# Kernel tuning notes

Hardware: AMD Instinct MI355X
Metric: run time of the kernel (lower is better)

The kernel has to match this reference:

```python
import jax, jax.numpy as jnp
import numpy as np

EPS = 1e-12

def _safe_norm(x, axis):
    return jnp.sqrt(jnp.sum(x * x, axis=axis) + EPS)

def _forward(z, pos, edge_index, batch, batch_size, emb, centers, gamma,
             fw1, fb1, fw2, fb2, uw1, ub1, uw2, ub2,
             ew1, eb1, ew2, eb2, dipole_w, nac_w,
             aw1, ab1, aw2, ab2, yw1, yb1, yw2, yb2):
    row, col = edge_index[0], edge_index[1]
    N = pos.shape[0]
    diff = pos[col] - pos[row]                    # (E,3)
    dist = _safe_norm(diff, axis=1)               # (E,)
    dirs = diff / (dist[:, None] + 1e-8)          # (E,3)
    rbf = jnp.exp(-gamma * (dist[:, None] - centers) ** 2)   # (E,R)
    s = emb[z]                                    # (N,F)
    v = jnp.zeros((N, s.shape[1], 3), s.dtype)    # (N,F,3)
    n_layers = fw1.shape[0]
    for l in range(n_layers):
        # filter MLP on RBF features -> 3 gates per edge
        phi = jax.nn.silu(rbf @ fw1[l] + fb1[l]) @ fw2[l] + fb2[l]   # (E,3F)
        phi_ss, phi_vv, phi_sv = jnp.split(phi, 3, axis=-1)
        sc = s[col]                                                    # gather (E,F)
        m_s = jax.ops.segment_sum(phi_ss * sc, row, num_segments=N)    # (N,F)
        m_v_e = (phi_vv[..., None] * v[col]
                 + phi_sv[..., None] * dirs[:, None, :] * sc[..., None])  # (E,F,3)
        m_v = jax.ops.segment_sum(m_v_e, row, num_segments=N)          # (N,F,3)
        v_norm = _safe_norm(m_v, axis=-1)                              # (N,F)
        upd = (jax.nn.silu(jnp.concatenate([s, m_s, v_norm], axis=-1) @ uw1[l] + ub1[l])
               @ uw2[l] + ub2[l])                                       # (N,3F)
        delta_s, alpha, beta = jnp.split(upd, 3, axis=-1)
        s = s + delta_s
        v = alpha[..., None] * v + beta[..., None] * m_v
    # energy heads (stacked over states S)
    h = jax.nn.silu(jnp.einsum('nf,sfg->nsg', s, ew1) + eb1)           # (N,S,F)
    e_atom = (jnp.einsum('nsg,sgo->nso', h, ew2) + eb2)[..., 0]        # (N,S)
    energies = jax.ops.segment_sum(e_atom, batch, num_segments=batch_size)  # (M,S)
    dipoles = jax.ops.segment_sum(jnp.einsum('nfk,f->nk', v, dipole_w), batch,
                                  num_segments=batch_size)             # (M,3)
    nac = jax.ops.segment_sum(jnp.einsum('nfk,pf->npk', v, nac_w), batch,
                              num_segments=batch_size)                 # (M,P,3)
    gaps = energies[:, 1:] - energies[:, :1]                           # (M,S-1)
    lam = jax.nn.silu(gaps @ aw1 + ab1) @ aw2 + ab2                    # (M,1)
    nac_mag = _safe_norm(nac, axis=-1)                                 # (M,P)
    phi_y = jax.nn.sigmoid(
        jax.nn.silu(jnp.concatenate([gaps, nac_mag], axis=1) @ yw1 + yb1) @ yw2 + yb2)  # (M,1)
    return energies, dipoles, nac, lam, phi_y

N, E, F, R, L, S, M, A = 20000, 320000, 128, 20, 3, 4, 1000, 100
P = S - 1

def setup_inputs() -> dict:
    key = jax.random.key(0)
    ks = jax.random.split(key, 32)
    w = lambda i, shape, sc=0.05: jax.random.normal(ks[i], shape, jnp.float32) * sc
    return {
        'z': jax.random.randint(ks[0], (N,), 0, A),
        'pos': jax.random.normal(ks[1], (N, 3), jnp.float32),
        'edge_index': jax.random.randint(ks[2], (2, E), 0, N),
        'batch': jnp.sort(jax.random.randint(ks[3], (N,), 0, M)),
        'batch_size': M,
        'emb': jax.random.normal(ks[4], (A, F), jnp.float32),
        'centers': jnp.linspace(0.0, 5.0, R),
        'gamma': jnp.ones((R,), jnp.float32),
        'fw1': w(5, (L, R, F)), 'fb1': jnp.zeros((L, F)),
        'fw2': w(6, (L, F, 3 * F)), 'fb2': jnp.zeros((L, 3 * F)),
        'uw1': w(7, (L, 3 * F, F)), 'ub1': jnp.zeros((L, F)),
        'uw2': w(8, (L, F, 3 * F)), 'ub2': jnp.zeros((L, 3 * F)),
        'ew1': w(9, (S, F, F)), 'eb1': jnp.zeros((S, F)),
        'ew2': w(10, (S, F, 1)), 'eb2': jnp.zeros((S, 1)),
        'dipole_w': jax.random.normal(ks[11], (F,), jnp.float32),
        'nac_w': jax.random.normal(ks[12], (P, F), jnp.float32),
        'aw1': w(13, (S - 1, 64)), 'ab1': jnp.zeros((64,)),
        'aw2': w(14, (64, 1)), 'ab2': jnp.zeros((1,)),
        'yw1': w(15, (S - 1 + P, 128)), 'yb1': jnp.zeros((128,)),
        'yw2': w(16, (128, 1)), 'yb2': jnp.zeros((1,)),
    }

def reference(z, pos, edge_index, batch, batch_size, emb, centers, gamma,
              fw1, fb1, fw2, fb2, uw1, ub1, uw2, ub2,
              ew1, eb1, ew2, eb2, dipole_w, nac_w,
              aw1, ab1, aw2, ab2, yw1, yb1, yw2, yb2):
    return _forward(z, pos, edge_index, batch, batch_size, emb, centers, gamma,
                    fw1, fb1, fw2, fb2, uw1, ub1, uw2, ub2,
                    ew1, eb1, ew2, eb2, dipole_w, nac_w,
                    aw1, ab1, aw2, ab2, yw1, yb1, yw2, yb2)
```

## Files before the change

kernel.cpp:

```cpp
#include <hip/hip_runtime.h>
#include <hip/hip_fp16.h>

#define FDIM 128
#define RDIM 20

#define TAB_T 2048
#define TAB_RANGE 12.0f

constexpr int TH = 256;

__device__ __forceinline__ float siluf(float x) { return x / (1.f + __expf(-x)); }

__device__ __forceinline__ void store_h4(__half* p, float a, float b, float c, float d) {
    __half h[4] = {__float2half(a), __float2half(b), __float2half(c), __float2half(d)};
    *(uint2*)p = *(uint2*)h;
}

__global__ void k_init(const int* __restrict__ z, const float* __restrict__ emb,
                       float* __restrict__ s, __half* __restrict__ s_h, int N) {
    int i = blockIdx.x * blockDim.x + threadIdx.x;
    if (i >= N * FDIM) return;
    int n = i >> 7, f = i & 127;
    float val = emb[z[n] * FDIM + f];
    s[i] = val;
    s_h[i] = __float2half(val);
}

__global__ void k_hist(const int* __restrict__ erow, int* __restrict__ cursor, int E) {
    int e = blockIdx.x * blockDim.x + threadIdx.x;
    if (e < E) atomicAdd(&cursor[erow[e]], 1);
}

__global__ __launch_bounds__(256) void k_scan1(const int* __restrict__ cursor,
                                               int* __restrict__ rowstart,
                                               int* __restrict__ bsum, int N) {
    __shared__ int sh[256];
    int tid = threadIdx.x;
    int idx = blockIdx.x * 256 + tid;
    int x = (idx < N) ? cursor[idx] : 0;
    sh[tid] = x;
    __syncthreads();
    #pragma unroll
    for (int off = 1; off < 256; off <<= 1) {
        int t = (tid >= off) ? sh[tid - off] : 0;
        __syncthreads();
        sh[tid] += t;
        __syncthreads();
    }
    if (idx < N) rowstart[idx] = sh[tid] - x;
    if (tid == 255) bsum[blockIdx.x] = sh[255];
}

__global__ __launch_bounds__(256) void k_scan2(int* __restrict__ bsum,
                                               int* __restrict__ rowstart, int nb, int N) {
    __shared__ int sh[256];
    __shared__ int carry;
    int tid = threadIdx.x;
    if (tid == 0) carry = 0;
    __syncthreads();
    for (int base = 0; base < nb; base += 256) {
        int idx = base + tid;
        int x = (idx < nb) ? bsum[idx] : 0;
        sh[tid] = x;
        __syncthreads();
        #pragma unroll
        for (int off = 1; off < 256; off <<= 1) {
            int t = (tid >= off) ? sh[tid - off] : 0;
            __syncthreads();
            sh[tid] += t;
            __syncthreads();
        }
        if (idx < nb) bsum[idx] = carry + sh[tid] - x;
        __syncthreads();
        if (tid == 0) carry += sh[255];
        __syncthreads();
    }
    if (tid == 0) rowstart[N] = carry;
}

__global__ __launch_bounds__(256) void k_scan3(int* __restrict__ rowstart,
                                               int* __restrict__ cursor,
                                               const int* __restrict__ bsum, int N) {
    int idx = blockIdx.x * 256 + threadIdx.x;
    if (idx < N) {
        int val = rowstart[idx] + bsum[blockIdx.x];
        rowstart[idx] = val;
        cursor[idx] = val;
    }
}

__global__ void k_fill(const int* __restrict__ erow, int* __restrict__ cursor,
                       int* __restrict__ esort, int E) {
    int e = blockIdx.x * blockDim.x + threadIdx.x;
    if (e < E) {
        int p = atomicAdd(&cursor[erow[e]], 1);
        esort[p] = e;
    }
}

__global__ void k_geom(const float* __restrict__ pos, const int* __restrict__ erow,
                       const int* __restrict__ ecol, const int* __restrict__ esort,
                       int2* __restrict__ geo_ci, float4* __restrict__ geo_wd,
                       float inv_step, int E) {
    int i = blockIdx.x * blockDim.x + threadIdx.x;
    if (i >= E) return;
    int e  = esort[i];
    int rw = erow[e], cl = ecol[e];
    float dx = pos[cl*3+0] - pos[rw*3+0];
    float dy = pos[cl*3+1] - pos[rw*3+1];
    float dz = pos[cl*3+2] - pos[rw*3+2];
    float dist = sqrtf(dx*dx + dy*dy + dz*dz + 1e-12f);
    float inv = 1.f / (dist + 1e-8f);
    float u = fminf(dist * inv_step, (float)TAB_T);
    int t0 = min((int)u, TAB_T - 1);
    geo_ci[i] = make_int2(cl, t0);
    geo_wd[i] = make_float4(u - (float)t0, dx*inv, dy*inv, dz*inv);
}

__global__ __launch_bounds__(TH) void k_table(
    const float* __restrict__ centers, const float* __restrict__ gamma,
    const float* __restrict__ fw1b, const float* __restrict__ fb1b,
    const float* __restrict__ fw2b, const float* __restrict__ fb2b,
    __half* __restrict__ tabb, float step)
{
    __shared__ float sh_rbf[32][RDIM];
    __shared__ float sh_ht[FDIM][33];
    __shared__ float sh_w[32][3 * FDIM + 4];

    const int l   = blockIdx.y;
    const float* fw1 = fw1b + (size_t)l * RDIM * FDIM;
    const float* fb1 = fb1b + (size_t)l * FDIM;
    const float* fw2 = fw2b + (size_t)l * FDIM * 3 * FDIM;
    const float* fb2 = fb2b + (size_t)l * 3 * FDIM;
    __half* tab = tabb + (size_t)l * (TAB_T + 1) * 384;

    const int p0  = blockIdx.x * 32;
    const int tid = threadIdx.x;

    for (int i = tid; i < 32 * RDIM; i += TH) {
        int p = i / RDIM, r = i - p * RDIM;
        float d = (float)(p0 + p) * step - centers[r];
        sh_rbf[p][r] = __expf(-gamma[r] * d * d);
    }
    __syncthreads();
    for (int i = tid; i < 32 * FDIM; i += TH) {
        int p = i >> 7, f = i & 127;
        float acc = fb1[f];
        #pragma unroll
        for (int r = 0; r < RDIM; ++r) acc += sh_rbf[p][r] * fw1[r * FDIM + f];
        sh_ht[f][p] = siluf(acc);
    }

    const int eq = tid & 7;
    const int fq = tid >> 3;
    const int f0 = fq * 4;

    float pg[3][4][4];
    #pragma unroll
    for (int g3 = 0; g3 < 3; ++g3)
        #pragma unroll
        for (int ee = 0; ee < 4; ++ee)
            #pragma unroll
            for (int i = 0; i < 4; ++i) pg[g3][ee][i] = fb2[g3 * FDIM + f0 + i];

    const int kkr = tid >> 3;
    const int t8  = tid & 7;
    for (int kc = 0; kc < 4; ++kc) {
        __syncthreads();
        #pragma unroll
        for (int j = 0; j < 12; ++j) {
            int g = (t8 * 12 + j) * 4;
            float4 w4 = *(const float4*)&fw2[(size_t)(kc * 32 + kkr) * (3 * FDIM) + g];
            *(float4*)&sh_w[kkr][g] = w4;
        }
        __syncthreads();
        #pragma unroll 4
        for (int kk = 0; kk < 32; ++kk) {
            float hv[4];
            #pragma unroll
            for (int ee = 0; ee < 4; ++ee) hv[ee] = sh_ht[kc * 32 + kk][4 * eq + ee];
            #pragma unroll
            for (int g3 = 0; g3 < 3; ++g3) {
                float4 w4 = *(const float4*)&sh_w[kk][g3 * FDIM + f0];
                #pragma unroll
                for (int ee = 0; ee < 4; ++ee) {
                    pg[g3][ee][0] += hv[ee] * w4.x;
                    pg[g3][ee][1] += hv[ee] * w4.y;
                    pg[g3][ee][2] += hv[ee] * w4.z;
                    pg[g3][ee][3] += hv[ee] * w4.w;
                }
            }
        }
    }

    #pragma unroll
    for (int ee = 0; ee < 4; ++ee) {
        int pt = p0 + 4 * eq + ee;
        if (pt <= TAB_T) {
            #pragma unroll
            for (int g3 = 0; g3 < 3; ++g3)
                store_h4(&tab[(size_t)pt * 384 + g3 * FDIM + f0],
                         pg[g3][ee][0], pg[g3][ee][1], pg[g3][ee][2], pg[g3][ee][3]);
        }
    }
}

__global__ __launch_bounds__(256) void k_repack(const __half* __restrict__ tab,
                                                __half2* __restrict__ tab2) {
    int l = blockIdx.y;
    const __half* t  = tab  + (size_t)l * (TAB_T + 1) * 384;
    __half2*      t2 = tab2 + (size_t)l * TAB_T * 384;
    int i = blockIdx.x * 256 + threadIdx.x;
    t2[i] = __halves2half2(t[i], t[i + 384]);
}

__global__ __launch_bounds__(128) void k_gather(
    const int* __restrict__ rowstart,
    const int2* __restrict__ geo_ci, const float4* __restrict__ geo_wd,
    const __half2* __restrict__ tab2, const __half* __restrict__ s_h,
    const __half* __restrict__ v_h,
    __half* __restrict__ m_s_h, __half* __restrict__ vnorm_h, __half* __restrict__ m_v_h,
    int withv, int N)
{
    __shared__ int   sh_col[32];
    __shared__ int   sh_t0[32];
    __shared__ float sh_w[32];
    __shared__ float sh_d0[32], sh_d1[32], sh_d2[32];

    const int n   = blockIdx.x;
    const int tid = threadIdx.x;
    const int lo  = rowstart[n], hi = rowstart[n + 1];

    float acc_s = 0.f, av0 = 0.f, av1 = 0.f, av2 = 0.f;

    for (int base = lo; base < hi; base += 32) {
        const int ne = min(32, hi - base);
        __syncthreads();
        if (tid < 32) {
            int idx = base + tid;
            if (tid < ne) {
                int2   ci = geo_ci[idx];
                float4 wd = geo_wd[idx];
                sh_col[tid] = ci.x; sh_t0[tid] = ci.y;
                sh_w[tid] = wd.x;
                sh_d0[tid] = wd.y; sh_d1[tid] = wd.z; sh_d2[tid] = wd.w;
            } else {
                sh_col[tid] = 0; sh_t0[tid] = 0; sh_w[tid] = 0.f;
                sh_d0[tid] = sh_d1[tid] = sh_d2[tid] = 0.f;
            }
        }
        __syncthreads();
        if (withv) {
            #pragma unroll 2
            for (int el = 0; el < ne; ++el) {
                int   cl = sh_col[el];
                int   t0 = sh_t0[el];
                float w  = sh_w[el];
                const __half2* t2 = tab2 + (size_t)t0 * 384 + tid;
                float2 pss2 = __half22float2(t2[0]);
                float2 pvv2 = __half22float2(t2[128]);
                float2 psv2 = __half22float2(t2[256]);
                float pss = pss2.x + w * (pss2.y - pss2.x);
                float pvv = pvv2.x + w * (pvv2.y - pvv2.x);
                float psv = psv2.x + w * (psv2.y - psv2.x);
                float sc = __half2float(s_h[(size_t)cl * FDIM + tid]);
                const __half* vp = v_h + (size_t)cl * 3 * FDIM + tid;
                float svs = psv * sc;
                acc_s += pss * sc;
                av0 += pvv * __half2float(vp[0])        + svs * sh_d0[el];
                av1 += pvv * __half2float(vp[FDIM])     + svs * sh_d1[el];
                av2 += pvv * __half2float(vp[2*FDIM])   + svs * sh_d2[el];
            }
        } else {
            #pragma unroll 2
            for (int el = 0; el < ne; ++el) {
                int   cl = sh_col[el];
                int   t0 = sh_t0[el];
                float w  = sh_w[el];
                const __half2* t2 = tab2 + (size_t)t0 * 384 + tid;
                float2 pss2 = __half22float2(t2[0]);
                float2 psv2 = __half22float2(t2[256]);
                float pss = pss2.x + w * (pss2.y - pss2.x);
                float psv = psv2.x + w * (psv2.y - psv2.x);
                float sc = __half2float(s_h[(size_t)cl * FDIM + tid]);
                float svs = psv * sc;
                acc_s += pss * sc;
                av0 += svs * sh_d0[el];
                av1 += svs * sh_d1[el];
                av2 += svs * sh_d2[el];
            }
        }
    }

    m_s_h[(size_t)n * FDIM + tid]  = __float2half(acc_s);
    vnorm_h[(size_t)n * FDIM + tid] = __float2half(sqrtf(av0*av0 + av1*av1 + av2*av2 + 1e-12f));
    __half* mh = m_v_h + (size_t)n * 3 * FDIM + tid;
    mh[0]      = __float2half(av0);
    mh[FDIM]   = __float2half(av1);
    mh[2*FDIM] = __float2half(av2);
}

__global__ __launch_bounds__(128) void k_mlp1(
    const __half* __restrict__ s_h, const __half* __restrict__ m_s_h,
    const __half* __restrict__ vnorm_h,
    const float* __restrict__ uw1, const float* __restrict__ ub1,
    __half* __restrict__ u1_h, int N)
{
    __shared__ float shA[16][36];
    __shared__ float shB[16][68];

    const int tid = threadIdx.x;
    const int n0  = blockIdx.x * 32;
    const int cb  = blockIdx.y * 64;
    const int tx  = tid & 15, ty = tid >> 4;
    const int cA  = tx * 4;
    const int r0  = ty * 4;
    const int rs  = tid >> 2;
    const int k4  = (tid & 3) * 4;

    float acc[4][4];
    {
        float4 b4 = *(const float4*)&ub1[cb + cA];
        #pragma unroll
        for (int i = 0; i < 4; ++i) {
            acc[i][0] = b4.x; acc[i][1] = b4.y; acc[i][2] = b4.z; acc[i][3] = b4.w;
        }
    }

    uint2 pa; float4 pb0, pb1;

#define MLP1_LOAD(kc) do { \
        pa = make_uint2(0u, 0u); \
        { int kg = (kc) * 16 + k4; int n = n0 + rs; \
          if (n < N) { \
              const __half* base; \
              if (kg < 128)      base = &s_h[(size_t)n * FDIM + kg]; \
              else if (kg < 256) base = &m_s_h[(size_t)n * FDIM + kg - 128]; \
              else               base = &vnorm_h[(size_t)n * FDIM + kg - 256]; \
              pa = *(const uint2*)base; } } \
        pb0 = *(const float4*)&uw1[(size_t)((kc)*16 + ty) * FDIM + cb + cA]; \
        pb1 = *(const float4*)&uw1[(size_t)((kc)*16 + 8 + ty) * FDIM + cb + cA]; \
    } while (0)

    MLP1_LOAD(0);
    for (int kc = 0; kc < 24; ++kc) {
        __syncthreads();
        {
            const __half* ph = (const __half*)&pa;
            shA[k4+0][rs] = __half2float(ph[0]); shA[k4+1][rs] = __half2float(ph[1]);
            shA[k4+2][rs] = __half2float(ph[2]); shA[k4+3][rs] = __half2float(ph[3]);
            *(float4*)&shB[ty][cA]     = pb0;
            *(float4*)&shB[8 + ty][cA] = pb1;
        }
        if (kc + 1 < 24) MLP1_LOAD(kc + 1);
        __syncthreads();
        #pragma unroll
        for (int kk = 0; kk < 16; ++kk) {
            float4 a4 = *(const float4*)&shA[kk][r0];
            float4 b4 = *(const float4*)&shB[kk][cA];
            float av[4] = {a4.x, a4.y, a4.z, a4.w};
            #pragma unroll
            for (int i = 0; i < 4; ++i) {
                acc[i][0] += av[i]*b4.x; acc[i][1] += av[i]*b4.y;
                acc[i][2] += av[i]*b4.z; acc[i][3] += av[i]*b4.w;
            }
        }
    }
#undef MLP1_LOAD

    #pragma unroll
    for (int i = 0; i < 4; ++i) {
        int n = n0 + r0 + i;
        if (n < N) {
            store_h4(&u1_h[(size_t)n * FDIM + cb + cA],
                     siluf(acc[i][0]), siluf(acc[i][1]), siluf(acc[i][2]), siluf(acc[i][3]));
        }
    }
}

__global__ __launch_bounds__(128) void k_mlp2(
    const __half* __restrict__ u1_h, const float* __restrict__ uw2, const float* __restrict__ ub2,
    float* __restrict__ s, __half* __restrict__ v_h, const __half* __restrict__ m_v_h,
    __half* __restrict__ s_h, int wmirror, int N)
{
    __shared__ float shU[32][132];
    __shared__ float shB[16][68];

    const int tid = threadIdx.x;
    const int n0  = blockIdx.x * 32;
    const int cb  = blockIdx.y * 64;
    const int tx  = tid & 15, ty = tid >> 4;
    const int cA  = tx * 4;
    const int r0  = ty * 4;

    #pragma unroll
    for (int it = 0; it < 4; ++it) {
        int idx = it * 128 + tid;
        int row = idx >> 4;
        int c8  = (idx & 15) * 8;
        int n = n0 + row;
        __half h[8];
        *(uint4*)h = make_uint4(0u,0u,0u,0u);
        if (n < N) *(uint4*)h = *(const uint4*)&u1_h[(size_t)n * FDIM + c8];
        #pragma unroll
        for (int j = 0; j < 8; ++j) shU[row][c8 + j] = __half2float(h[j]);
    }

    float4 pb0, pb1;
#define MLP2_LOADB(g, kc) do { \
        pb0 = *(const float4*)&uw2[(size_t)((kc)*16 + ty) * (3*FDIM) + (g) * FDIM + cb + cA]; \
        pb1 = *(const float4*)&uw2[(size_t)((kc)*16 + 8 + ty) * (3*FDIM) + (g) * FDIM + cb + cA]; \
    } while (0)

    MLP2_LOADB(0, 0);
    float alpha[4][4];

    for (int g = 0; g < 3; ++g) {
        float acc2[4][4];
        {
            float4 b4 = *(const float4*)&ub2[g * FDIM + cb + cA];
            #pragma unroll
            for (int i = 0; i < 4; ++i) {
                acc2[i][0]=b4.x; acc2[i][1]=b4.y; acc2[i][2]=b4.z; acc2[i][3]=b4.w;
            }
        }
        for (int kc = 0; kc < 8; ++kc) {
            __syncthreads();
            *(float4*)&shB[ty][cA]     = pb0;
            *(float4*)&shB[8 + ty][cA] = pb1;
            if (kc + 1 < 8)      MLP2_LOADB(g, kc + 1);
            else if (g + 1 < 3)  MLP2_LOADB(g + 1, 0);
            __syncthreads();
            #pragma unroll
            for (int kk = 0; kk < 16; ++kk) {
                int col = kc * 16 + kk;
                float4 b4 = *(const float4*)&shB[kk][cA];
                #pragma unroll
                for (int i = 0; i < 4; ++i) {
                    float uv = shU[r0 + i][col];
                    acc2[i][0] += uv*b4.x; acc2[i][1] += uv*b4.y;
                    acc2[i][2] += uv*b4.z; acc2[i][3] += uv*b4.w;
                }
            }
        }

        if (g == 0) {
            #pragma unroll
            for (int i = 0; i < 4; ++i) {
                int n = n0 + r0 + i;
                if (n < N) {
                    float4 s0 = *(const float4*)&s[(size_t)n * FDIM + cb + cA];
                    s0.x += acc2[i][0]; s0.y += acc2[i][1]; s0.z += acc2[i][2]; s0.w += acc2[i][3];
                    *(float4*)&s[(size_t)n * FDIM + cb + cA] = s0;
                    if (wmirror)
                        store_h4(&s_h[(size_t)n * FDIM + cb + cA], s0.x, s0.y, s0.z, s0.w);
                }
            }
        } else if (g == 1) {
            #pragma unroll
            for (int i = 0; i < 4; ++i)
                #pragma unroll
                for (int j = 0; j < 4; ++j) alpha[i][j] = acc2[i][j];
        } else {
            #pragma unroll
            for (int i = 0; i < 4; ++i) {
                int n = n0 + r0 + i;
                if (n < N) {
                    #pragma unroll
                    for (int k = 0; k < 3; ++k) {
                        __half* vhp = v_h + ((size_t)n * 3 + k) * FDIM + cb + cA;
                        const __half* mp = m_v_h + ((size_t)n * 3 + k) * FDIM + cb + cA;
                        __half vh[4], mh[4];
                        *(uint2*)vh = *(const uint2*)vhp;
                        *(uint2*)mh = *(const uint2*)mp;
                        float nv[4];
                        #pragma unroll
                        for (int j = 0; j < 4; ++j)
                            nv[j] = alpha[i][j] * __half2float(vh[j])
                                  + acc2[i][j] * __half2float(mh[j]);
                        store_h4(vhp, nv[0], nv[1], nv[2], nv[3]);
                    }
                }
            }
        }
    }
#undef MLP2_LOADB
}

__global__ __launch_bounds__(256) void k_energy2(
    const float* __restrict__ ew1, const float* __restrict__ eb1,
    const float* __restrict__ ew2, const float* __restrict__ eb2,
    const float* __restrict__ s, const int* __restrict__ batch,
    float* __restrict__ energies, int N, int S)
{
    __shared__ float shA[16][68];
    __shared__ float shB[16][132];

    const int tid = threadIdx.x;
    const int n0  = blockIdx.x * 64;
    const int st  = blockIdx.y;
    const int tx  = tid & 15, ty = tid >> 4;
    const int cA  = tx * 4, cB = 64 + tx * 4;
    const int r0  = ty * 4;
    const int rs  = tid >> 2;
    const int k4  = (tid & 3) * 4;

    float acc[4][8];
    {
        float4 bA = *(const float4*)&eb1[st * FDIM + cA];
        float4 bB = *(const float4*)&eb1[st * FDIM + cB];
        #pragma unroll
        for (int i = 0; i < 4; ++i) {
            acc[i][0]=bA.x; acc[i][1]=bA.y; acc[i][2]=bA.z; acc[i][3]=bA.w;
            acc[i][4]=bB.x; acc[i][5]=bB.y; acc[i][6]=bB.z; acc[i][7]=bB.w;
        }
    }

    for (int kc = 0; kc < 8; ++kc) {
        __syncthreads();
        {
            int kg = kc * 16 + k4;
            int n  = n0 + rs;
            float4 a = make_float4(0.f, 0.f, 0.f, 0.f);
            if (n < N) a = *(const float4*)&s[(size_t)n * FDIM + kg];
            shA[k4+0][rs] = a.x; shA[k4+1][rs] = a.y; shA[k4+2][rs] = a.z; shA[k4+3][rs] = a.w;
        }
        #pragma unroll
        for (int i = 0; i < 2; ++i) {
            int idx = tid + i * 256;
            int kk = idx >> 5;
            int c4 = (idx & 31) * 4;
            *(float4*)&shB[kk][c4] =
                *(const float4*)&ew1[(size_t)st * FDIM * FDIM + (size_t)(kc*16+kk) * FDIM + c4];
        }
        __syncthreads();
        #pragma unroll
        for (int kk = 0; kk < 16; ++kk) {
            float4 a4 = *(const float4*)&shA[kk][r0];
            float4 b0 = *(const float4*)&shB[kk][cA];
            float4 b1 = *(const float4*)&shB[kk][cB];
            float av[4] = {a4.x, a4.y, a4.z, a4.w};
            #pragma unroll
            for (int i = 0; i < 4; ++i) {
                acc[i][0] += av[i]*b0.x; acc[i][1] += av[i]*b0.y;
                acc[i][2] += av[i]*b0.z; acc[i][3] += av[i]*b0.w;
                acc[i][4] += av[i]*b1.x; acc[i][5] += av[i]*b1.y;
                acc[i][6] += av[i]*b1.z; acc[i][7] += av[i]*b1.w;
            }
        }
    }

    float4 wA = *(const float4*)&ew2[st * FDIM + cA];
    float4 wB = *(const float4*)&ew2[st * FDIM + cB];
    float p[4];
    #pragma unroll
    for (int i = 0; i < 4; ++i) {
        p[i]  = siluf(acc[i][0])*wA.x + siluf(acc[i][1])*wA.y
              + siluf(acc[i][2])*wA.z + siluf(acc[i][3])*wA.w;
        p[i] += siluf(acc[i][4])*wB.x + siluf(acc[i][5])*wB.y
              + siluf(acc[i][6])*wB.z + siluf(acc[i][7])*wB.w;
    }
    #pragma unroll
    for (int m = 1; m <= 8; m <<= 1) {
        #pragma unroll
        for (int i = 0; i < 4; ++i) p[i] += __shfl_xor(p[i], m, 64);
    }
    if (tx == 0) {
        float b2 = eb2[st];
        #pragma unroll
        for (int i = 0; i < 4; ++i) {
            int n = n0 + r0 + i;
            if (n < N) atomicAdd(&energies[batch[n] * S + st], p[i] + b2);
        }
    }
}

__global__ void k_vec(const __half* __restrict__ v_h, const float* __restrict__ dipole_w,
                      const float* __restrict__ nac_w, const int* __restrict__ batch,
                      float* __restrict__ dipoles, float* __restrict__ nac, int N)
{
    int n = blockIdx.x * 4 + (threadIdx.x >> 6);
    int lane = threadIdx.x & 63;
    if (n >= N) return;
    float pd[3] = {0.f, 0.f, 0.f};
    float pn[3][3] = {{0.f}};
    const __half* vb = v_h + (size_t)n * 3 * FDIM;
    for (int f = lane; f < FDIM; f += 64) {
        float v0 = __half2float(vb[f]);
        float v1 = __half2float(vb[FDIM + f]);
        float v2 = __half2float(vb[2*FDIM + f]);
        float wd = dipole_w[f];
        pd[0] += wd * v0; pd[1] += wd * v1; pd[2] += wd * v2;
        #pragma unroll
        for (int p = 0; p < 3; ++p) {
            float wn = nac_w[p * FDIM + f];
            pn[p][0] += wn * v0; pn[p][1] += wn * v1; pn[p][2] += wn * v2;
        }
    }
    #pragma unroll
    for (int d = 32; d > 0; d >>= 1) {
        #pragma unroll
        for (int k = 0; k < 3; ++k) pd[k] += __shfl_down(pd[k], d, 64);
        #pragma unroll
        for (int p = 0; p < 3; ++p)
            #pragma unroll
            for (int k = 0; k < 3; ++k) pn[p][k] += __shfl_down(pn[p][k], d, 64);
    }
    if (lane == 0) {
        int m = batch[n];
        #pragma unroll
        for (int k = 0; k < 3; ++k) atomicAdd(&dipoles[m * 3 + k], pd[k]);
        #pragma unroll
        for (int p = 0; p < 3; ++p)
            #pragma unroll
            for (int k = 0; k < 3; ++k) atomicAdd(&nac[(m * 3 + p) * 3 + k], pn[p][k]);
    }
}

__global__ __launch_bounds__(128) void k_heads(
    const float* __restrict__ aw1, const float* __restrict__ ab1,
    const float* __restrict__ aw2, const float* __restrict__ ab2,
    const float* __restrict__ yw1, const float* __restrict__ yb1,
    const float* __restrict__ yw2, const float* __restrict__ yb2,
    const float* __restrict__ energies, const float* __restrict__ nac,
    float* __restrict__ lam, float* __restrict__ phi_y, int M, int S)
{
    __shared__ float sh_in[8];
    __shared__ float sh_red[2];
    int m = blockIdx.x;
    if (m >= M) return;
    int tid = threadIdx.x;
    if (tid == 0) {
        float e0 = energies[m * S];
        for (int j = 0; j < 3; ++j) sh_in[j] = energies[m * S + 1 + j] - e0;
        for (int p = 0; p < 3; ++p) {
            float a = nac[(m * 3 + p) * 3 + 0];
            float b = nac[(m * 3 + p) * 3 + 1];
            float c = nac[(m * 3 + p) * 3 + 2];
            sh_in[3 + p] = sqrtf(a*a + b*b + c*c + 1e-12f);
        }
    }
    __syncthreads();
    float pa = 0.f;
    if (tid < 64) {
        float h = ab1[tid];
        #pragma unroll
        for (int j = 0; j < 3; ++j) h += sh_in[j] * aw1[j * 64 + tid];
        pa = siluf(h) * aw2[tid];
    }
    float h2 = yb1[tid];
    #pragma unroll
    for (int j = 0; j < 6; ++j) h2 += sh_in[j] * yw1[j * 128 + tid];
    float py = siluf(h2) * yw2[tid];
    #pragma unroll
    for (int d = 32; d > 0; d >>= 1) {
        pa += __shfl_down(pa, d, 64);
        py += __shfl_down(py, d, 64);
    }
    int wid = tid >> 6, lane = tid & 63;
    if (lane == 0) sh_red[wid] = py;
    __syncthreads();
    if (tid == 0) {
        lam[m] = pa + ab2[0];
        float yt = sh_red[0] + sh_red[1] + yb2[0];
        phi_y[m] = 1.f / (1.f + __expf(-yt));
    }
}

extern "C" void kernel_launch(void* const* d_in, const int* in_sizes, int n_in,
                              void* d_out, int out_size, void* d_ws, size_t ws_size,
                              hipStream_t stream)
{
    const int*   z        = (const int*)  d_in[0];
    const float* pos      = (const float*)d_in[1];
    const int*   eidx     = (const int*)  d_in[2];
    const int*   batch    = (const int*)  d_in[3];
    const float* emb      = (const float*)d_in[5];
    const float* centers  = (const float*)d_in[6];
    const float* gamma    = (const float*)d_in[7];
    const float* fw1      = (const float*)d_in[8];
    const float* fb1      = (const float*)d_in[9];
    const float* fw2      = (const float*)d_in[10];
    const float* fb2      = (const float*)d_in[11];
    const float* uw1      = (const float*)d_in[12];
    const float* ub1      = (const float*)d_in[13];
    const float* uw2      = (const float*)d_in[14];
    const float* ub2      = (const float*)d_in[15];
    const float* ew1      = (const float*)d_in[16];
    const float* eb1      = (const float*)d_in[17];
    const float* ew2      = (const float*)d_in[18];
    const float* eb2      = (const float*)d_in[19];
    const float* dipole_w = (const float*)d_in[20];
    const float* nac_w    = (const float*)d_in[21];
    const float* aw1      = (const float*)d_in[22];
    const float* ab1      = (const float*)d_in[23];
    const float* aw2      = (const float*)d_in[24];
    const float* ab2      = (const float*)d_in[25];
    const float* yw1      = (const float*)d_in[26];
    const float* yb1      = (const float*)d_in[27];
    const float* yw2      = (const float*)d_in[28];
    const float* yb2      = (const float*)d_in[29];

    const int N = in_sizes[0];
    const int E = in_sizes[2] / 2;
    const int S = in_sizes[19];
    const int P = in_sizes[21] / FDIM;
    const int L = in_sizes[9] / FDIM;
    const int M = out_size / (S + 3 + P * 3 + 2);

    const size_t NF = (size_t)N * FDIM;
    float*   s       = (float*)d_ws;
    __half*  s_h     = (__half*)(s + NF);
    __half*  v_h     = s_h + NF;
    __half*  m_s_h   = v_h + 3 * NF;
    __half*  vnorm_h = m_s_h + NF;
    __half*  m_v_h   = vnorm_h + NF;
    __half*  u1_hb   = m_v_h + 3 * NF;
    __half*  tab     = u1_hb + NF;
    __half2* tab2    = (__half2*)(tab + (size_t)L * (TAB_T + 1) * 384);
    float4*  geo_wd  = (float4*)(tab2 + (size_t)L * TAB_T * 384);
    int2*    geo_ci  = (int2*)(geo_wd + E);
    int* rowstart = (int*)(geo_ci + E);
    int* cursor   = rowstart + (N + 1);
    int* esort    = cursor + N;
    int* bsum     = esort + E;

    float* out      = (float*)d_out;
    float* energies = out;
    float* dipoles  = energies + (size_t)M * S;
    float* nac      = dipoles  + (size_t)M * 3;
    float* lam      = nac      + (size_t)M * P * 3;
    float* phi_y    = lam      + M;

    const int* erow = eidx;
    const int* ecol = eidx + E;

    const float step = TAB_RANGE / (float)TAB_T;
    const float inv_step = (float)TAB_T / TAB_RANGE;
    const int NB  = (N + 63) / 64;
    const int NB2 = (N + 31) / 32;
    const int NSB = (N + 255) / 256;

    hipMemsetAsync(d_out, 0, (size_t)out_size * sizeof(float), stream);
    hipMemsetAsync(cursor, 0, (size_t)N * sizeof(int), stream);
    hipMemsetAsync(v_h, 0, 3 * NF * sizeof(__half), stream);
    k_hist<<<(E + 255) / 256, 256, 0, stream>>>(erow, cursor, E);
    k_scan1<<<NSB, 256, 0, stream>>>(cursor, rowstart, bsum, N);
    k_scan2<<<1, 256, 0, stream>>>(bsum, rowstart, NSB, N);
    k_scan3<<<NSB, 256, 0, stream>>>(rowstart, cursor, bsum, N);
    k_fill<<<(E + 255) / 256, 256, 0, stream>>>(erow, cursor, esort, E);
    k_geom<<<(E + 255) / 256, 256, 0, stream>>>(pos, erow, ecol, esort, geo_ci, geo_wd, inv_step, E);
    k_init<<<(N * FDIM + 255) / 256, 256, 0, stream>>>(z, emb, s, s_h, N);

    const int tab_blocks = (TAB_T + 1 + 31) / 32;
    k_table<<<dim3(tab_blocks, L), TH, 0, stream>>>(centers, gamma, fw1, fb1, fw2, fb2, tab, step);
    k_repack<<<dim3(TAB_T * 384 / 256, L), 256, 0, stream>>>(tab, tab2);

    for (int l = 0; l < L; ++l) {
        const __half2* tab2_l = tab2 + (size_t)l * TAB_T * 384;
        k_gather<<<N, 128, 0, stream>>>(
            rowstart, geo_ci, geo_wd, tab2_l, s_h, v_h,
            m_s_h, vnorm_h, m_v_h, (l > 0) ? 1 : 0, N);
        k_mlp1<<<dim3(NB2, 2), 128, 0, stream>>>(
            s_h, m_s_h, vnorm_h,
            uw1 + (size_t)l * 3 * FDIM * FDIM, ub1 + (size_t)l * FDIM, u1_hb, N);
        k_mlp2<<<dim3(NB2, 2), 128, 0, stream>>>(
            u1_hb, uw2 + (size_t)l * FDIM * 3 * FDIM, ub2 + (size_t)l * 3 * FDIM,
            s, v_h, m_v_h, s_h, (l + 1 < L) ? 1 : 0, N);
    }

    k_energy2<<<dim3(NB, S), 256, 0, stream>>>(ew1, eb1, ew2, eb2, s, batch, energies, N, S);
    k_vec<<<(N + 3) / 4, 256, 0, stream>>>(v_h, dipole_w, nac_w, batch, dipoles, nac, N);
    k_heads<<<M, 128, 0, stream>>>(aw1, ab1, aw2, ab2, yw1, yb1, yw2, yb2,
                                   energies, nac, lam, phi_y, M, S);
}
```

Measured before the change: 557.6 us.

## Map one wavefront per node in gather and broadcast edge metadata via readlane

The gather kernel now assigns one 64-lane wavefront per destination node, each lane handling two features, with four nodes per 256-thread block instead of one 128-thread block per node. Edge metadata is loaded into registers and broadcast with readlane instead of being staged through shared memory, which removes both __syncthreads barriers. Table, s and v reads are widened to half2/uint2 vector loads. This cuts block count and barrier overhead, but the loop is scalar-dependent on readlane and the manual unroll pragma is gone.

```diff
diff --git a/kernel.cpp b/kernel.cpp
--- a/kernel.cpp
+++ b/kernel.cpp
@@ -14,6 +14,10 @@
 __device__ __forceinline__ void store_h4(__half* p, float a, float b, float c, float d) {
     __half h[4] = {__float2half(a), __float2half(b), __float2half(c), __float2half(d)};
     *(uint2*)p = *(uint2*)h;
+}
+
+__device__ __forceinline__ float bcast_f(float x, int l) {
+    return __int_as_float(__builtin_amdgcn_readlane(__float_as_int(x), l));
 }
 
 __global__ void k_init(const int* __restrict__ z, const float* __restrict__ emb,
@@ -214,7 +218,7 @@
     t2[i] = __halves2half2(t[i], t[i + 384]);
 }
 
-__global__ __launch_bounds__(128) void k_gather(
+__global__ __launch_bounds__(256) void k_gather(
     const int* __restrict__ rowstart,
     const int2* __restrict__ geo_ci, const float4* __restrict__ geo_wd,
     const __half2* __restrict__ tab2, const __half* __restrict__ s_h,
@@ -222,82 +226,103 @@
     __half* __restrict__ m_s_h, __half* __restrict__ vnorm_h, __half* __restrict__ m_v_h,
     int withv, int N)
 {
-    __shared__ int   sh_col[32];
-    __shared__ int   sh_t0[32];
-    __shared__ float sh_w[32];
-    __shared__ float sh_d0[32], sh_d1[32], sh_d2[32];
-
-    const int n   = blockIdx.x;
-    const int tid = threadIdx.x;
-    const int lo  = rowstart[n], hi = rowstart[n + 1];
-
-    float acc_s = 0.f, av0 = 0.f, av1 = 0.f, av2 = 0.f;
+    const int wid  = threadIdx.x >> 6;
+    const int lane = threadIdx.x & 63;
+    const int n    = blockIdx.x * 4 + wid;
+    if (n >= N) return;
+    const int lo = rowstart[n], hi = rowstart[n + 1];
+    const int f2 = lane * 2;
+
+    float ms0 = 0.f, ms1 = 0.f;
+    float a00 = 0.f, a01 = 0.f, a10 = 0.f, a11 = 0.f, a20 = 0.f, a21 = 0.f;
 
     for (int base = lo; base < hi; base += 32) {
         const int ne = min(32, hi - base);
-        __syncthreads();
-        if (tid < 32) {
-            int idx = base + tid;
-            if (tid < ne) {
-                int2   ci = geo_ci[idx];
-                float4 wd = geo_wd[idx];
-                sh_col[tid] = ci.x; sh_t0[tid] = ci.y;
-                sh_w[tid] = wd.x;
-                sh_d0[tid] = wd.y; sh_d1[tid] = wd.z; sh_d2[tid] = wd.w;
-            } else {
-                sh_col[tid] = 0; sh_t0[tid] = 0; sh_w[tid] = 0.f;
-                sh_d0[tid] = sh_d1[tid] = sh_d2[tid] = 0.f;
-            }
-        }
-        __syncthreads();
+        int colr = 0, t0r = 0;
+        float wr = 0.f, d0r = 0.f, d1r = 0.f, d2r = 0.f;
+        if (lane < ne) {
+            int2   ci = geo_ci[base + lane];
+            float4 wd = geo_wd[base + lane];
+            colr = ci.x; t0r = ci.y;
+            wr = wd.x; d0r = wd.y; d1r = wd.z; d2r = wd.w;
+        }
         if (withv) {
-            #pragma unroll 2
             for (int el = 0; el < ne; ++el) {
-                int   cl = sh_col[el];
-                int   t0 = sh_t0[el];
-                float w  = sh_w[el];
-                const __half2* t2 = tab2 + (size_t)t0 * 384 + tid;
-                float2 pss2 = __half22float2(t2[0]);
-                float2 pvv2 = __half22float2(t2[128]);
-                float2 psv2 = __half22float2(t2[256]);
-                float pss = pss2.x + w * (pss2.y - pss2.x);
-                float pvv = pvv2.x + w * (pvv2.y - pvv2.x);
-                float psv = psv2.x + w * (psv2.y - psv2.x);
-                float sc = __half2float(s_h[(size_t)cl * FDIM + tid]);
-                const __half* vp = v_h + (size_t)cl * 3 * FDIM + tid;
-                float svs = psv * sc;
-                acc_s += pss * sc;
-                av0 += pvv * __half2float(vp[0])        + svs * sh_d0[el];
-                av1 += pvv * __half2float(vp[FDIM])     + svs * sh_d1[el];
-                av2 += pvv * __half2float(vp[2*FDIM])   + svs * sh_d2[el];
+                const int   cl = __builtin_amdgcn_readlane(colr, el);
+                const int   tt = __builtin_amdgcn_readlane(t0r, el);
+                const float w  = bcast_f(wr, el);
+                const float e0 = bcast_f(d0r, el);
+                const float e1 = bcast_f(d1r, el);
+                const float e2 = bcast_f(d2r, el);
+
+                const __half2* tb = tab2 + (size_t)tt * 384 + f2;
+                uint2 uss = *(const uint2*)(tb);
+                uint2 uvv = *(const uint2*)(tb + 128);
+                uint2 usv = *(const uint2*)(tb + 256);
+                float2 ssA = __half22float2(*(const __half2*)&uss.x);
+                float2 ssB = __half22float2(*(const __half2*)&uss.y);
+                float2 vvA = __half22float2(*(const __half2*)&uvv.x);
+                float2 vvB = __half22float2(*(const __half2*)&uvv.y);
+                float2 svA = __half22float2(*(const __half2*)&usv.x);
+                float2 svB = __half22float2(*(const __half2*)&usv.y);
+                float pss0 = ssA.x + w * (ssA.y - ssA.x);
+                float pss1 = ssB.x + w * (ssB.y - ssB.x);
+                float pvv0 = vvA.x + w * (vvA.y - vvA.x);
+                float pvv1 = vvB.x + w * (vvB.y - vvB.x);
+                float psv0 = svA.x + w * (svA.y - svA.x);
+                float psv1 = svB.x + w * (svB.y - svB.x);
+
+                float2 sc = __half22float2(*(const __half2*)&s_h[(size_t)cl * FDIM + f2]);
+                const __half* vp = v_h + (size_t)cl * 3 * FDIM + f2;
+                float2 v0 = __half22float2(*(const __half2*)&vp[0]);
+                float2 v1 = __half22float2(*(const __half2*)&vp[FDIM]);
+                float2 v2 = __half22float2(*(const __half2*)&vp[2*FDIM]);
+
+                float svs0 = psv0 * sc.x, svs1 = psv1 * sc.y;
+                ms0 += pss0 * sc.x;  ms1 += pss1 * sc.y;
+                a00 += pvv0 * v0.x + svs0 * e0;  a01 += pvv1 * v0.y + svs1 * e0;
+                a10 += pvv0 * v1.x + svs0 * e1;  a11 += pvv1 * v1.y + svs1 * e1;
+                a20 += pvv0 * v2.x + svs0 * e2;  a21 += pvv1 * v2.y + svs1 * e2;
             }
         } else {
-            #pragma unroll 2
             for (int el = 0; el < ne; ++el) {
-                int   cl = sh_col[el];
-                int   t0 = sh_t0[el];
-                float w  = sh_w[el];
-                const __half2* t2 = tab2 + (size_t)t0 * 384 + tid;
-                float2 pss2 = __half22float2(t2[0]);
-                float2 psv2 = __half22float2(t2[256]);
-                float pss = pss2.x + w * (pss2.y - pss2.x);
-                float psv = psv2.x + w * (psv2.y - psv2.x);
-                float sc = __half2float(s_h[(size_t)cl * FDIM + tid]);
-                float svs = psv * sc;
-                acc_s += pss * sc;
-                av0 += svs * sh_d0[el];
-                av1 += svs * sh_d1[el];
-                av2 += svs * sh_d2[el];
+                const int   cl = __builtin_amdgcn_readlane(colr, el);
+                const int   tt = __builtin_amdgcn_readlane(t0r, el);
+                const float w  = bcast_f(wr, el);
+                const float e0 = bcast_f(d0r, el);
+                const float e1 = bcast_f(d1r, el);
+                const float e2 = bcast_f(d2r, el);
+
+                const __half2* tb = tab2 + (size_t)tt * 384 + f2;
+                uint2 uss = *(const uint2*)(tb);
+                uint2 usv = *(const uint2*)(tb + 256);
+                float2 ssA = __half22float2(*(const __half2*)&uss.x);
+                float2 ssB = __half22float2(*(const __half2*)&uss.y);
+                float2 svA = __half22float2(*(const __half2*)&usv.x);
+                float2 svB = __half22float2(*(const __half2*)&usv.y);
+                float pss0 = ssA.x + w * (ssA.y - ssA.x);
+                float pss1 = ssB.x + w * (ssB.y - ssB.x);
+                float psv0 = svA.x + w * (svA.y - svA.x);
+                float psv1 = svB.x + w * (svB.y - svB.x);
+
+                float2 sc = __half22float2(*(const __half2*)&s_h[(size_t)cl * FDIM + f2]);
+                float svs0 = psv0 * sc.x, svs1 = psv1 * sc.y;
+                ms0 += pss0 * sc.x;  ms1 += pss1 * sc.y;
+                a00 += svs0 * e0;  a01 += svs1 * e0;
+                a10 += svs0 * e1;  a11 += svs1 * e1;
+                a20 += svs0 * e2;  a21 += svs1 * e2;
             }
         }
     }
 
-    m_s_h[(size_t)n * FDIM + tid]  = __float2half(acc_s);
-    vnorm_h[(size_t)n * FDIM + tid] = __float2half(sqrtf(av0*av0 + av1*av1 + av2*av2 + 1e-12f));
-    __half* mh = m_v_h + (size_t)n * 3 * FDIM + tid;
-    mh[0]      = __float2half(av0);
-    mh[FDIM]   = __float2half(av1);
-    mh[2*FDIM] = __float2half(av2);
+    *(__half2*)&m_s_h[(size_t)n * FDIM + f2] = __floats2half2_rn(ms0, ms1);
+    float vn0 = sqrtf(a00*a00 + a10*a10 + a20*a20 + 1e-12f);
+    float vn1 = sqrtf(a01*a01 + a11*a11 + a21*a21 + 1e-12f);
+    *(__half2*)&vnorm_h[(size_t)n * FDIM + f2] = __floats2half2_rn(vn0, vn1);
+    __half* mh = m_v_h + (size_t)n * 3 * FDIM + f2;
+    *(__half2*)&mh[0]      = __floats2half2_rn(a00, a01);
+    *(__half2*)&mh[FDIM]   = __floats2half2_rn(a10, a11);
+    *(__half2*)&mh[2*FDIM] = __floats2half2_rn(a20, a21);
 }
 
 __global__ __launch_bounds__(128) void k_mlp1(
@@ -758,7 +783,7 @@
 
     for (int l = 0; l < L; ++l) {
         const __half2* tab2_l = tab2 + (size_t)l * TAB_T * 384;
-        k_gather<<<N, 128, 0, stream>>>(
+        k_gather<<<(N + 3) / 4, 256, 0, stream>>>(
             rowstart, geo_ci, geo_wd, tab2_l, s_h, v_h,
             m_s_h, vnorm_h, m_v_h, (l > 0) ? 1 : 0, N);
         k_mlp1<<<dim3(NB2, 2), 128, 0, stream>>>(
```

New measurement: 563.2 us. Within noise of the previous version (+1.0%).

## Use packed fp16 dot2 for node update MLP matmuls with prepacked weights

Applied to the files above, without the earlier changes.

Adds a pre-pass that converts the update MLP weights into k-paired half2 words, and rewrites the two node MLP GEMM kernels to keep activations and weights as packed half2 in shared memory, accumulating with v_dot2_f32_f16. This halves weight bandwidth and shared-memory traffic, removes half-to-float conversions, and halves the FMA instruction count. Weights now lose precision to fp16, and a few extra packing launches are added per call.

```diff
diff --git a/kernel.cpp b/kernel.cpp
--- a/kernel.cpp
+++ b/kernel.cpp
@@ -14,6 +14,13 @@
 __device__ __forceinline__ void store_h4(__half* p, float a, float b, float c, float d) {
     __half h[4] = {__float2half(a), __float2half(b), __float2half(c), __float2half(d)};
     *(uint2*)p = *(uint2*)h;
+}
+
+typedef _Float16 h2v __attribute__((ext_vector_type(2)));
+__device__ __forceinline__ float fdot2u(unsigned int a, unsigned int b, float c) {
+    union { unsigned int u; h2v h; } ua, ub;
+    ua.u = a; ub.u = b;
+    return __builtin_amdgcn_fdot2(ua.h, ub.h, c, false);
 }
 
 __global__ void k_init(const int* __restrict__ z, const float* __restrict__ emb,
@@ -24,6 +31,16 @@
     float val = emb[z[n] * FDIM + f];
     s[i] = val;
     s_h[i] = __float2half(val);
+}
+
+__global__ void k_pack(const float* __restrict__ src, unsigned int* __restrict__ dst,
+                       int C, int total) {
+    int i = blockIdx.x * 256 + threadIdx.x;
+    if (i >= total) return;
+    int kp = i / C, c = i - kp * C;
+    __half2 h = __halves2half2(__float2half(src[(2*kp) * C + c]),
+                               __float2half(src[(2*kp+1) * C + c]));
+    dst[i] = *(unsigned int*)&h;
 }
 
 __global__ void k_hist(const int* __restrict__ erow, int* __restrict__ cursor, int E) {
@@ -303,11 +320,12 @@
 __global__ __launch_bounds__(128) void k_mlp1(
     const __half* __restrict__ s_h, const __half* __restrict__ m_s_h,
     const __half* __restrict__ vnorm_h,
-    const float* __restrict__ uw1, const float* __restrict__ ub1,
+    const unsigned int* __restrict__ uw1p,
+    const float* __restrict__ ub1,
     __half* __restrict__ u1_h, int N)
 {
-    __shared__ float shA[16][36];
-    __shared__ float shB[16][68];
+    __shared__ unsigned int shA2[8][36];
+    __shared__ unsigned int shB2[8][68];
 
     const int tid = threadIdx.x;
     const int n0  = blockIdx.x * 32;
@@ -316,7 +334,7 @@
     const int cA  = tx * 4;
     const int r0  = ty * 4;
     const int rs  = tid >> 2;
-    const int k4  = (tid & 3) * 4;
+    const int kp0 = (tid & 3) * 2;
 
     float acc[4][4];
     {
@@ -327,42 +345,39 @@
         }
     }
 
-    uint2 pa; float4 pb0, pb1;
+    uint2 pa; uint4 pb;
 
 #define MLP1_LOAD(kc) do { \
         pa = make_uint2(0u, 0u); \
-        { int kg = (kc) * 16 + k4; int n = n0 + rs; \
+        { int kg = (kc) * 16 + (tid & 3) * 4; int n = n0 + rs; \
           if (n < N) { \
               const __half* base; \
               if (kg < 128)      base = &s_h[(size_t)n * FDIM + kg]; \
               else if (kg < 256) base = &m_s_h[(size_t)n * FDIM + kg - 128]; \
               else               base = &vnorm_h[(size_t)n * FDIM + kg - 256]; \
               pa = *(const uint2*)base; } } \
-        pb0 = *(const float4*)&uw1[(size_t)((kc)*16 + ty) * FDIM + cb + cA]; \
-        pb1 = *(const float4*)&uw1[(size_t)((kc)*16 + 8 + ty) * FDIM + cb + cA]; \
+        pb = *(const uint4*)&uw1p[(size_t)((kc)*8 + ty) * FDIM + cb + 4*tx]; \
     } while (0)
 
     MLP1_LOAD(0);
     for (int kc = 0; kc < 24; ++kc) {
         __syncthreads();
-        {
-            const __half* ph = (const __half*)&pa;
-            shA[k4+0][rs] = __half2float(ph[0]); shA[k4+1][rs] = __half2float(ph[1]);
-            shA[k4+2][rs] = __half2float(ph[2]); shA[k4+3][rs] = __half2float(ph[3]);
-            *(float4*)&shB[ty][cA]     = pb0;
-            *(float4*)&shB[8 + ty][cA] = pb1;
-        }
+        shA2[kp0][rs]     = pa.x;
+        shA2[kp0 + 1][rs] = pa.y;
+        *(uint4*)&shB2[ty][4*tx] = pb;
         if (kc + 1 < 24) MLP1_LOAD(kc + 1);
         __syncthreads();
         #pragma unroll
-        for (int kk = 0; kk < 16; ++kk) {
-            float4 a4 = *(const float4*)&shA[kk][r0];
-            float4 b4 = *(const float4*)&shB[kk][cA];
-            float av[4] = {a4.x, a4.y, a4.z, a4.w};
+        for (int kp = 0; kp < 8; ++kp) {
+            unsigned int b0 = shB2[kp][cA+0], b1 = shB2[kp][cA+1];
+            unsigned int b2 = shB2[kp][cA+2], b3 = shB2[kp][cA+3];
             #pragma unroll
             for (int i = 0; i < 4; ++i) {
-                acc[i][0] += av[i]*b4.x; acc[i][1] += av[i]*b4.y;
-                acc[i][2] += av[i]*b4.z; acc[i][3] += av[i]*b4.w;
+                unsigned int ai = shA2[kp][r0 + i];
+                acc[i][0] = fdot2u(ai, b0, acc[i][0]);
+                acc[i][1] = fdot2u(ai, b1, acc[i][1]);
+                acc[i][2] = fdot2u(ai, b2, acc[i][2]);
+                acc[i][3] = fdot2u(ai, b3, acc[i][3]);
             }
         }
     }
@@ -379,12 +394,14 @@
 }
 
 __global__ __launch_bounds__(128) void k_mlp2(
-    const __half* __restrict__ u1_h, const float* __restrict__ uw2, const float* __restrict__ ub2,
+    const __half* __restrict__ u1_h,
+    const unsigned int* __restrict__ uw2p,
+    const float* __restrict__ ub2,
     float* __restrict__ s, __half* __restrict__ v_h, const __half* __restrict__ m_v_h,
     __half* __restrict__ s_h, int wmirror, int N)
 {
-    __shared__ float shU[32][132];
-    __shared__ float shB[16][68];
+    __shared__ unsigned int shU2[64][33];
+    __shared__ unsigned int shB2[8][68];
 
     const int tid = threadIdx.x;
     const int n0  = blockIdx.x * 32;
@@ -399,17 +416,18 @@
         int row = idx >> 4;
         int c8  = (idx & 15) * 8;
         int n = n0 + row;
-        __half h[8];
-        *(uint4*)h = make_uint4(0u,0u,0u,0u);
-        if (n < N) *(uint4*)h = *(const uint4*)&u1_h[(size_t)n * FDIM + c8];
-        #pragma unroll
-        for (int j = 0; j < 8; ++j) shU[row][c8 + j] = __half2float(h[j]);
-    }
-
-    float4 pb0, pb1;
+        uint4 u = make_uint4(0u,0u,0u,0u);
+        if (n < N) u = *(const uint4*)&u1_h[(size_t)n * FDIM + c8];
+        int kpb = c8 >> 1;
+        shU2[kpb + 0][row] = u.x;
+        shU2[kpb + 1][row] = u.y;
+        shU2[kpb + 2][row] = u.z;
+        shU2[kpb + 3][row] = u.w;
+    }
+
+    uint4 pb;
 #define MLP2_LOADB(g, kc) do { \
-        pb0 = *(const float4*)&uw2[(size_t)((kc)*16 + ty) * (3*FDIM) + (g) * FDIM + cb + cA]; \
-        pb1 = *(const float4*)&uw2[(size_t)((kc)*16 + 8 + ty) * (3*FDIM) + (g) * FDIM + cb + cA]; \
+        pb = *(const uint4*)&uw2p[(size_t)((kc)*8 + ty) * (3*FDIM) + (g) * FDIM + cb + 4*tx]; \
     } while (0)
 
     MLP2_LOADB(0, 0);
@@ -426,20 +444,22 @@
         }
         for (int kc = 0; kc < 8; ++kc) {
             __syncthreads();
-            *(float4*)&shB[ty][cA]     = pb0;
-            *(float4*)&shB[8 + ty][cA] = pb1;
+            *(uint4*)&shB2[ty][4*tx] = pb;
             if (kc + 1 < 8)      MLP2_LOADB(g, kc + 1);
             else if (g + 1 < 3)  MLP2_LOADB(g + 1, 0);
             __syncthreads();
             #pragma unroll
-            for (int kk = 0; kk < 16; ++kk) {
-                int col = kc * 16 + kk;
-                float4 b4 = *(const float4*)&shB[kk][cA];
+            for (int kp = 0; kp < 8; ++kp) {
+                int kpg = kc * 8 + kp;
+                unsigned int b0 = shB2[kp][cA+0], b1 = shB2[kp][cA+1];
+                unsigned int b2 = shB2[kp][cA+2], b3 = shB2[kp][cA+3];
                 #pragma unroll
                 for (int i = 0; i < 4; ++i) {
-                    float uv = shU[r0 + i][col];
-                    acc2[i][0] += uv*b4.x; acc2[i][1] += uv*b4.y;
-                    acc2[i][2] += uv*b4.z; acc2[i][3] += uv*b4.w;
+                    unsigned int uv = shU2[kpg][r0 + i];
+                    acc2[i][0] = fdot2u(uv, b0, acc2[i][0]);
+                    acc2[i][1] = fdot2u(uv, b1, acc2[i][1]);
+                    acc2[i][2] = fdot2u(uv, b2, acc2[i][2]);
+                    acc2[i][3] = fdot2u(uv, b3, acc2[i][3]);
                 }
             }
         }
@@ -716,7 +736,9 @@
     __half*  vnorm_h = m_s_h + NF;
     __half*  m_v_h   = vnorm_h + NF;
     __half*  u1_hb   = m_v_h + 3 * NF;
-    __half*  tab     = u1_hb + NF;
+    unsigned int* uw1p = (unsigned int*)(u1_hb + NF);
+    unsigned int* uw2p = uw1p + (size_t)L * 192 * 128;
+    __half*  tab     = (__half*)(uw2p + (size_t)L * 64 * 384);
     __half2* tab2    = (__half2*)(tab + (size_t)L * (TAB_T + 1) * 384);
     float4*  geo_wd  = (float4*)(tab2 + (size_t)L * TAB_T * 384);
     int2*    geo_ci  = (int2*)(geo_wd + E);
@@ -752,6 +774,13 @@
     k_geom<<<(E + 255) / 256, 256, 0, stream>>>(pos, erow, ecol, esort, geo_ci, geo_wd, inv_step, E);
     k_init<<<(N * FDIM + 255) / 256, 256, 0, stream>>>(z, emb, s, s_h, N);
 
+    for (int l = 0; l < L; ++l) {
+        k_pack<<<(192*128 + 255) / 256, 256, 0, stream>>>(
+            uw1 + (size_t)l * 3 * FDIM * FDIM, uw1p + (size_t)l * 192 * 128, 128, 192 * 128);
+        k_pack<<<(64*384 + 255) / 256, 256, 0, stream>>>(
+            uw2 + (size_t)l * FDIM * 3 * FDIM, uw2p + (size_t)l * 64 * 384, 384, 64 * 384);
+    }
+
     const int tab_blocks = (TAB_T + 1 + 31) / 32;
     k_table<<<dim3(tab_blocks, L), TH, 0, stream>>>(centers, gamma, fw1, fb1, fw2, fb2, tab, step);
     k_repack<<<dim3(TAB_T * 384 / 256, L), 256, 0, stream>>>(tab, tab2);
@@ -763,9 +792,9 @@
             m_s_h, vnorm_h, m_v_h, (l > 0) ? 1 : 0, N);
         k_mlp1<<<dim3(NB2, 2), 128, 0, stream>>>(
             s_h, m_s_h, vnorm_h,
-            uw1 + (size_t)l * 3 * FDIM * FDIM, ub1 + (size_t)l * FDIM, u1_hb, N);
+            uw1p + (size_t)l * 192 * 128, ub1 + (size_t)l * FDIM, u1_hb, N);
         k_mlp2<<<dim3(NB2, 2), 128, 0, stream>>>(
-            u1_hb, uw2 + (size_t)l * FDIM * 3 * FDIM, ub2 + (size_t)l * 3 * FDIM,
+            u1_hb, uw2p + (size_t)l * 64 * 384, ub2 + (size_t)l * 3 * FDIM,
             s, v_h, m_v_h, s_h, (l + 1 < L) ? 1 : 0, N);
     }
 
```

After: 512.4 us. -8.1%, faster.
